# Optimization experiments

Hardware: AMD Instinct MI355X
Metric: run time of the kernel (lower is better)

## Reference

```python
import jax, jax.numpy as jnp
import numpy as np

NEG_SLOPE = 0.2  # PyG GATConv default leaky_relu slope


def gat_layer(x, src, dst, W, a_src, a_dst, bias, heads, out_ch, concat):
    """One GATConv layer (PyG semantics, shared lin for src/dst).
    x: [N, F_in]; src/dst: [E] int; W: [F_in, heads*out_ch];
    a_src/a_dst: [heads, out_ch]; bias: [heads*out_ch] or [out_ch]."""
    N = x.shape[0]
    h = (x @ W).reshape(N, heads, out_ch)              # [N, H, C]
    al_s = jnp.sum(h * a_src, axis=-1)                 # [N, H]
    al_d = jnp.sum(h * a_dst, axis=-1)                 # [N, H]
    e = jax.nn.leaky_relu(al_s[src] + al_d[dst], NEG_SLOPE)  # [E, H]
    # segment softmax over incoming edges of each destination node
    m = jax.ops.segment_max(e, dst, num_segments=N)
    m = jnp.where(jnp.isfinite(m), m, 0.0)             # nodes w/o edges
    ex = jnp.exp(e - m[dst])
    denom = jax.ops.segment_sum(ex, dst, num_segments=N)
    alpha = ex / denom[dst]                            # [E, H]; denom>0 via self-loops
    out = jax.ops.segment_sum(alpha[:, :, None] * h[src], dst, num_segments=N)  # [N,H,C]
    out = out.reshape(N, heads * out_ch) if concat else out.mean(axis=1)
    return out + bias


def setup_inputs() -> dict:
    key = jax.random.key(0)
    ks = jax.random.split(key, 10)
    N, E, F_in, Ch = 50000, 800000, 5, 64
    glorot = lambda k, shp: jax.random.uniform(
        k, shp, jnp.float32, -1.0, 1.0) * np.sqrt(6.0 / (shp[0] + shp[-1]))
    return {
        "x": jax.random.normal(ks[0], (N, F_in), jnp.float32),
        "edge_index": jax.random.randint(ks[1], (2, E), 0, N, jnp.int32),
        "W1": glorot(ks[2], (F_in, 4 * Ch)),
        "a_src1": glorot(ks[3], (4, Ch)),
        "a_dst1": glorot(ks[4], (4, Ch)),
        "b1": jnp.zeros((4 * Ch,), jnp.float32),
        "W2": glorot(ks[5], (4 * Ch, Ch)),
        "a_src2": glorot(ks[6], (1, Ch)),
        "a_dst2": glorot(ks[7], (1, Ch)),
        "b2": jnp.zeros((Ch,), jnp.float32),
    }


def reference(x, edge_index, W1, a_src1, a_dst1, b1, W2, a_src2, a_dst2, b2):
    N = x.shape[0]
    loops = jnp.arange(N, dtype=edge_index.dtype)      # PyG adds self-loops by default
    src = jnp.concatenate([edge_index[0], loops])
    dst = jnp.concatenate([edge_index[1], loops])
    h = gat_layer(x, src, dst, W1, a_src1, a_dst1, b1, heads=4, out_ch=64, concat=True)
    h = jax.nn.relu(h)
    h = gat_layer(h, src, dst, W2, a_src2, a_dst2, b2, heads=1, out_ch=64, concat=False)
    return h.mean(axis=0)                              # [64]
```

## Files before the change

### kernel.cpp

```cpp
#include <hip/hip_runtime.h>
#include <hip/hip_bf16.h>

#define NEG_SLOPE 0.2f

typedef __attribute__((ext_vector_type(8))) short short8;
typedef __attribute__((ext_vector_type(4))) float f32x4;

__device__ __forceinline__ float wave_sum64(float v) {
#pragma unroll
    for (int off = 32; off >= 1; off >>= 1) v += __shfl_xor(v, off, 64);
    return v;
}

__device__ __forceinline__ float bf2f(unsigned short u) {
    return __uint_as_float((unsigned int)u << 16);
}

__device__ __forceinline__ unsigned short f2bf(float f) {
    __hip_bfloat16 hb = __float2bfloat16(f);
    return *reinterpret_cast<unsigned short*>(&hb);
}

__global__ __launch_bounds__(256) void kb1_deg(
    const int* __restrict__ ei, int E, int Etot, int* __restrict__ deg) {
    int e = blockIdx.x * 256 + threadIdx.x;
    if (e >= Etot) return;
    int dst = (e < E) ? ei[E + e] : e - E;
    atomicAdd(&deg[dst], 1);
}

__global__ __launch_bounds__(256) void kb2_alloc(
    const int* __restrict__ deg, int N, int* __restrict__ counter,
    int* __restrict__ row_ptr, int* __restrict__ row_end,
    int* __restrict__ row_cur) {
    int n = blockIdx.x * 256 + threadIdx.x;
    int lane = threadIdx.x & 63;
    int d = (n < N) ? deg[n] : 0;
    int x = d;
#pragma unroll
    for (int off = 1; off < 64; off <<= 1) {
        int y = __shfl_up(x, off, 64);
        if (lane >= off) x += y;
    }
    int total = __shfl(x, 63, 64);
    int base = 0;
    if (lane == 63) base = atomicAdd(counter, total);
    base = __shfl(base, 63, 64);
    if (n < N) {
        int beg = base + x - d;
        row_ptr[n] = beg; row_cur[n] = beg; row_end[n] = beg + d;
    }
}

__global__ __launch_bounds__(256) void kb3_scatter(
    const int* __restrict__ ei, int E, int Etot,
    int* __restrict__ row_cur, int* __restrict__ csr_src) {
    int e = blockIdx.x * 256 + threadIdx.x;
    if (e >= Etot) return;
    int src, dst;
    if (e < E) { src = ei[e]; dst = ei[E + e]; }
    else       { src = dst = e - E; }
    int pos = atomicAdd(&row_cur[dst], 1);
    csr_src[pos] = src;
}

__global__ __launch_bounds__(256) void kw_pack(
    const float* __restrict__ W2, unsigned short* __restrict__ W2t) {
    int i = blockIdx.x * 256 + threadIdx.x;
    if (i >= 64 * 256) return;
    int c = i >> 8, k = i & 255;
    W2t[c * 256 + k] = f2bf(W2[k * 64 + c]);
}

__global__ __launch_bounds__(256) void k1_node1(
    const float* __restrict__ x, const float* __restrict__ W1,
    const float* __restrict__ a_src1, const float* __restrict__ a_dst1,
    unsigned short* __restrict__ h1b, float* __restrict__ al_s1,
    float* __restrict__ al_d1, int N) {
    int n = blockIdx.x;
    if (n >= N) return;
    int t = threadIdx.x;
    float h = 0.f;
#pragma unroll
    for (int k = 0; k < 5; ++k) h = fmaf(x[n * 5 + k], W1[k * 256 + t], h);
    int head = t >> 6, ch = t & 63;
    h1b[(size_t)n * 256 + ch * 4 + head] = f2bf(h);
    float s = wave_sum64(h * a_src1[t]);
    float d = wave_sum64(h * a_dst1[t]);
    if (ch == 0) {
        al_s1[n * 4 + head] = s;
        al_d1[n * 4 + head] = d;
    }
}

__global__ __launch_bounds__(256) void k2a_wts(
    const int* __restrict__ csr_src, const int* __restrict__ row_ptr,
    const int* __restrict__ row_end, const float* __restrict__ al_s1,
    const float* __restrict__ al_d1, float* __restrict__ ew,
    float* __restrict__ denom1, int N) {
    int wave = threadIdx.x >> 6, lane = threadIdx.x & 63;
    int n = blockIdx.x * 4 + wave;
    if (n >= N) return;
    int beg = row_ptr[n], end = row_end[n];
    const float4 ad = *reinterpret_cast<const float4*>(&al_d1[n * 4]);
    float d0 = 0.f, d1 = 0.f, d2 = 0.f, d3 = 0.f;
    for (int base = beg; base < end; base += 64) {
        int e = base + lane;
        if (e < end) {
            int src = csr_src[e];
            const float4 as = *reinterpret_cast<const float4*>(&al_s1[src * 4]);
            float v0 = as.x + ad.x, v1 = as.y + ad.y, v2 = as.z + ad.z, v3 = as.w + ad.w;
            v0 = v0 > 0.f ? v0 : NEG_SLOPE * v0;
            v1 = v1 > 0.f ? v1 : NEG_SLOPE * v1;
            v2 = v2 > 0.f ? v2 : NEG_SLOPE * v2;
            v3 = v3 > 0.f ? v3 : NEG_SLOPE * v3;
            float4 ex;
            ex.x = __expf(v0); ex.y = __expf(v1); ex.z = __expf(v2); ex.w = __expf(v3);
            *reinterpret_cast<float4*>(&ew[(size_t)e * 4]) = ex;
            d0 += ex.x; d1 += ex.y; d2 += ex.z; d3 += ex.w;
        }
    }
    d0 = wave_sum64(d0); d1 = wave_sum64(d1);
    d2 = wave_sum64(d2); d3 = wave_sum64(d3);
    if (lane == 0) {
        float4 dn = {d0, d1, d2, d3};
        *reinterpret_cast<float4*>(&denom1[n * 4]) = dn;
    }
}

__global__ __launch_bounds__(256) void k2b_gather1(
    const int* __restrict__ csr_src, const int* __restrict__ row_ptr,
    const int* __restrict__ row_end, const unsigned short* __restrict__ h1b,
    const float* __restrict__ ew, const float* __restrict__ denom1,
    const float* __restrict__ b1, unsigned short* __restrict__ x2b, int N) {
    int wave = threadIdx.x >> 6, lane = threadIdx.x & 63;
    int n = blockIdx.x * 4 + wave;
    if (n >= N) return;
    int beg = row_ptr[n], end = row_end[n];
    float a0 = 0.f, a1 = 0.f, a2 = 0.f, a3 = 0.f;
    for (int base = beg; base < end; base += 64) {
        int nn = min(64, end - base);
        int srcv = (base + lane < end) ? csr_src[base + lane] : 0;
        for (int i = 0; i < nn; ++i) {
            int src = __shfl(srcv, i, 64);
            const float4 w = *reinterpret_cast<const float4*>(&ew[(size_t)(base + i) * 4]);
            const ushort4 u = *reinterpret_cast<const ushort4*>(
                &h1b[(size_t)src * 256 + lane * 4]);
            a0 = fmaf(w.x, bf2f(u.x), a0);
            a1 = fmaf(w.y, bf2f(u.y), a1);
            a2 = fmaf(w.z, bf2f(u.z), a2);
            a3 = fmaf(w.w, bf2f(u.w), a3);
        }
    }
    const float4 dn = *reinterpret_cast<const float4*>(&denom1[n * 4]);
    unsigned short* xo = &x2b[(size_t)n * 256];
    float r;
    r = a0 / dn.x + b1[0 * 64 + lane]; xo[0 * 64 + lane] = f2bf(r > 0.f ? r : 0.f);
    r = a1 / dn.y + b1[1 * 64 + lane]; xo[1 * 64 + lane] = f2bf(r > 0.f ? r : 0.f);
    r = a2 / dn.z + b1[2 * 64 + lane]; xo[2 * 64 + lane] = f2bf(r > 0.f ? r : 0.f);
    r = a3 / dn.w + b1[3 * 64 + lane]; xo[3 * 64 + lane] = f2bf(r > 0.f ? r : 0.f);
}

__global__ __launch_bounds__(256) void k3_mfma(
    const unsigned short* __restrict__ x2b, const unsigned short* __restrict__ W2t,
    const float* __restrict__ a_src2, const float* __restrict__ a_dst2,
    float* __restrict__ h2, float* __restrict__ al_s2, float* __restrict__ al_d2,
    int N) {
    int w = threadIdx.x >> 6, l = threadIdx.x & 63;
    int m0 = blockIdx.x * 64 + w * 16;
    if (m0 >= N) return;
    int lr = l & 15, lg = l >> 4;

    short8 b0[8], b1f[8], b2f[8], b3f[8];
#pragma unroll
    for (int kk = 0; kk < 8; ++kk) {
        b0[kk]  = *reinterpret_cast<const short8*>(&W2t[(0 * 16 + lr) * 256 + kk * 32 + lg * 8]);
        b1f[kk] = *reinterpret_cast<const short8*>(&W2t[(1 * 16 + lr) * 256 + kk * 32 + lg * 8]);
        b2f[kk] = *reinterpret_cast<const short8*>(&W2t[(2 * 16 + lr) * 256 + kk * 32 + lg * 8]);
        b3f[kk] = *reinterpret_cast<const short8*>(&W2t[(3 * 16 + lr) * 256 + kk * 32 + lg * 8]);
    }
    short8 a[8];
#pragma unroll
    for (int kk = 0; kk < 8; ++kk)
        a[kk] = *reinterpret_cast<const short8*>(&x2b[(size_t)(m0 + lr) * 256 + kk * 32 + lg * 8]);

    f32x4 acc0 = {0.f, 0.f, 0.f, 0.f}, acc1 = acc0, acc2 = acc0, acc3 = acc0;
#pragma unroll
    for (int kk = 0; kk < 8; ++kk) {
        acc0 = __builtin_amdgcn_mfma_f32_16x16x32_bf16(a[kk], b0[kk],  acc0, 0, 0, 0);
        acc1 = __builtin_amdgcn_mfma_f32_16x16x32_bf16(a[kk], b1f[kk], acc1, 0, 0, 0);
        acc2 = __builtin_amdgcn_mfma_f32_16x16x32_bf16(a[kk], b2f[kk], acc2, 0, 0, 0);
        acc3 = __builtin_amdgcn_mfma_f32_16x16x32_bf16(a[kk], b3f[kk], acc3, 0, 0, 0);
    }

#pragma unroll
    for (int j = 0; j < 4; ++j) {
        float* hr = &h2[(size_t)(m0 + lg * 4 + j) * 64];
        hr[0 * 16 + lr] = acc0[j];
        hr[1 * 16 + lr] = acc1[j];
        hr[2 * 16 + lr] = acc2[j];
        hr[3 * 16 + lr] = acc3[j];
    }

    float sA0 = a_src2[0 * 16 + lr], sA1 = a_src2[1 * 16 + lr];
    float sA2 = a_src2[2 * 16 + lr], sA3 = a_src2[3 * 16 + lr];
    float sD0 = a_dst2[0 * 16 + lr], sD1 = a_dst2[1 * 16 + lr];
    float sD2 = a_dst2[2 * 16 + lr], sD3 = a_dst2[3 * 16 + lr];
    float p0 = acc0[0] * sA0 + acc1[0] * sA1 + acc2[0] * sA2 + acc3[0] * sA3;
    float p1 = acc0[1] * sA0 + acc1[1] * sA1 + acc2[1] * sA2 + acc3[1] * sA3;
    float p2 = acc0[2] * sA0 + acc1[2] * sA1 + acc2[2] * sA2 + acc3[2] * sA3;
    float p3 = acc0[3] * sA0 + acc1[3] * sA1 + acc2[3] * sA2 + acc3[3] * sA3;
    float q0 = acc0[0] * sD0 + acc1[0] * sD1 + acc2[0] * sD2 + acc3[0] * sD3;
    float q1 = acc0[1] * sD0 + acc1[1] * sD1 + acc2[1] * sD2 + acc3[1] * sD3;
    float q2 = acc0[2] * sD0 + acc1[2] * sD1 + acc2[2] * sD2 + acc3[2] * sD3;
    float q3 = acc0[3] * sD0 + acc1[3] * sD1 + acc2[3] * sD2 + acc3[3] * sD3;
#pragma unroll
    for (int off = 1; off <= 8; off <<= 1) {
        p0 += __shfl_xor(p0, off, 64); p1 += __shfl_xor(p1, off, 64);
        p2 += __shfl_xor(p2, off, 64); p3 += __shfl_xor(p3, off, 64);
        q0 += __shfl_xor(q0, off, 64); q1 += __shfl_xor(q1, off, 64);
        q2 += __shfl_xor(q2, off, 64); q3 += __shfl_xor(q3, off, 64);
    }
    if (lr == 0) {
        int r0 = m0 + lg * 4;
        al_s2[r0 + 0] = p0; al_s2[r0 + 1] = p1; al_s2[r0 + 2] = p2; al_s2[r0 + 3] = p3;
        al_d2[r0 + 0] = q0; al_d2[r0 + 1] = q1; al_d2[r0 + 2] = q2; al_d2[r0 + 3] = q3;
    }
}

__global__ __launch_bounds__(256) void k4a_wts(
    const int* __restrict__ csr_src, const int* __restrict__ row_ptr,
    const int* __restrict__ row_end, const float* __restrict__ al_s2,
    const float* __restrict__ al_d2, float* __restrict__ ew2,
    float* __restrict__ denom2, int N) {
    int wave = threadIdx.x >> 6, lane = threadIdx.x & 63;
    int n = blockIdx.x * 4 + wave;
    if (n >= N) return;
    int beg = row_ptr[n], end = row_end[n];
    float ad = al_d2[n];
    float dsum = 0.f;
    for (int base = beg; base < end; base += 64) {
        int e = base + lane;
        if (e < end) {
            int src = csr_src[e];
            float v = al_s2[src] + ad;
            v = v > 0.f ? v : NEG_SLOPE * v;
            float ex = __expf(v);
            ew2[e] = ex;
            dsum += ex;
        }
    }
    dsum = wave_sum64(dsum);
    if (lane == 0) denom2[n] = dsum;
}

__global__ __launch_bounds__(256) void k4b_gather2(
    const int* __restrict__ csr_src, const int* __restrict__ row_ptr,
    const int* __restrict__ row_end, const float* __restrict__ h2,
    const float* __restrict__ ew2, const float* __restrict__ denom2,
    float* __restrict__ o2, int N) {
    int wave = threadIdx.x >> 6, lane = threadIdx.x & 63;
    int n = blockIdx.x * 4 + wave;
    if (n >= N) return;
    int beg = row_ptr[n], end = row_end[n];
    float a = 0.f;
    for (int base = beg; base < end; base += 64) {
        int nn = min(64, end - base);
        int srcv = (base + lane < end) ? csr_src[base + lane] : 0;
        for (int i = 0; i < nn; ++i) {
            int src = __shfl(srcv, i, 64);
            float w = ew2[base + i];
            a = fmaf(w, h2[(size_t)src * 64 + lane], a);
        }
    }
    o2[(size_t)n * 64 + lane] = a / denom2[n];
}

__global__ __launch_bounds__(64) void k5_final(
    const float* __restrict__ o2, const float* __restrict__ b2,
    float* __restrict__ out, int N) {
    int lane = threadIdx.x;
    float acc = 0.f;
    for (int n = blockIdx.x; n < N; n += gridDim.x)
        acc += o2[(size_t)n * 64 + lane];
    float v = acc * (1.f / (float)N);
    if (blockIdx.x == 0) v += b2[lane];
    atomicAdd(&out[lane], v);
}

extern "C" void kernel_launch(void* const* d_in, const int* in_sizes, int n_in,
                              void* d_out, int out_size, void* d_ws, size_t ws_size,
                              hipStream_t stream) {
    const float* x   = (const float*)d_in[0];
    const int*   ei  = (const int*)d_in[1];
    const float* W1  = (const float*)d_in[2];
    const float* as1 = (const float*)d_in[3];
    const float* ad1 = (const float*)d_in[4];
    const float* b1  = (const float*)d_in[5];
    const float* W2  = (const float*)d_in[6];
    const float* as2 = (const float*)d_in[7];
    const float* ad2 = (const float*)d_in[8];
    const float* b2  = (const float*)d_in[9];
    float* out = (float*)d_out;

    const int F_in = in_sizes[2] / 256;
    const int N = in_sizes[0] / F_in;
    const int E = in_sizes[1] / 2;
    const int Etot = E + N;

    unsigned short* h1b = (unsigned short*)d_ws;
    unsigned short* x2b = h1b + (size_t)N * 256;
    float* h2    = (float*)(x2b + (size_t)N * 256);
    float* al_s1 = h2 + (size_t)N * 64;
    float* al_d1 = al_s1 + (size_t)N * 4;
    float* ew    = al_d1 + (size_t)N * 4;
    float* denom1= ew + (size_t)Etot * 4;
    unsigned short* W2t = (unsigned short*)(denom1 + (size_t)N * 4);
    int* deg     = (int*)(W2t + 64 * 256);
    int* row_cur = deg + N;
    int* row_ptr = row_cur + N;
    int* row_end = row_ptr + N;
    int* counter = row_end + N;
    int* csr_src = counter + 1;
    float* o2    = (float*)h1b;
    float* al_s2 = al_s1;
    float* al_d2 = al_d1;
    float* ew2   = ew;
    float* denom2= denom1;

    hipMemsetAsync(deg, 0, (size_t)N * sizeof(int), stream);
    hipMemsetAsync(counter, 0, sizeof(int), stream);
    hipMemsetAsync(out, 0, 64 * sizeof(float), stream);

    kb1_deg    <<<(Etot + 255) / 256, 256, 0, stream>>>(ei, E, Etot, deg);
    kb2_alloc  <<<(N + 255) / 256, 256, 0, stream>>>(deg, N, counter, row_ptr, row_end, row_cur);
    kb3_scatter<<<(Etot + 255) / 256, 256, 0, stream>>>(ei, E, Etot, row_cur, csr_src);
    kw_pack    <<<64, 256, 0, stream>>>(W2, W2t);

    k1_node1   <<<N, 256, 0, stream>>>(x, W1, as1, ad1, h1b, al_s1, al_d1, N);
    k2a_wts    <<<(N + 3) / 4, 256, 0, stream>>>(csr_src, row_ptr, row_end, al_s1, al_d1, ew, denom1, N);
    k2b_gather1<<<(N + 3) / 4, 256, 0, stream>>>(csr_src, row_ptr, row_end, h1b, ew, denom1, b1, x2b, N);
    k3_mfma    <<<(N + 63) / 64, 256, 0, stream>>>(x2b, W2t, as2, ad2, h2, al_s2, al_d2, N);
    k4a_wts    <<<(N + 3) / 4, 256, 0, stream>>>(csr_src, row_ptr, row_end, al_s2, al_d2, ew2, denom2, N);
    k4b_gather2<<<(N + 3) / 4, 256, 0, stream>>>(csr_src, row_ptr, row_end, h2, ew2, denom2, o2, N);
    k5_final   <<<256, 64, 0, stream>>>(o2, b2, out, N);
}
```

Baseline: 442.5 us.

## Aggregate raw 5-dim inputs before W1 projection and store h2 in bf16

Layer 1 is reordered by linearity: attention logits come from precomputed W1·a vectors, and the softmax-weighted sum runs over the 5-feature input x instead of the 256-wide h1. The projection through W1 is applied once per destination node. This removes the h1 materialization, the per-edge weight buffer and one gather kernel, shrinking per-edge traffic from 512 bytes to 20. Layer-2 features h2 are also stored as bf16 to halve gather bandwidth, at some cost in precision.

Result: faster. 400.4 us (-9.5%).

```diff
diff --git a/kernel.cpp b/kernel.cpp
--- a/kernel.cpp
+++ b/kernel.cpp
@@ -72,38 +72,64 @@
     W2t[c * 256 + k] = f2bf(W2[k * 64 + c]);
 }
 
-__global__ __launch_bounds__(256) void k1_node1(
-    const float* __restrict__ x, const float* __restrict__ W1,
-    const float* __restrict__ a_src1, const float* __restrict__ a_dst1,
-    unsigned short* __restrict__ h1b, float* __restrict__ al_s1,
+__global__ __launch_bounds__(256) void kpre(
+    const float* __restrict__ W1, const float* __restrict__ a_src1,
+    const float* __restrict__ a_dst1, float* __restrict__ Wa_s,
+    float* __restrict__ Wa_d) {
+    int t = threadIdx.x;
+    int h = t >> 6;
+    float a_s = a_src1[t], a_d = a_dst1[t];
+#pragma unroll
+    for (int f = 0; f < 5; ++f) {
+        float w = W1[f * 256 + t];
+        float ps = wave_sum64(w * a_s);
+        float pd = wave_sum64(w * a_d);
+        if ((t & 63) == 0) { Wa_s[f * 4 + h] = ps; Wa_d[f * 4 + h] = pd; }
+    }
+}
+
+__global__ __launch_bounds__(256) void k1p(
+    const float* __restrict__ x, const float* __restrict__ Wa_s,
+    const float* __restrict__ Wa_d, float* __restrict__ al_s1,
     float* __restrict__ al_d1, int N) {
-    int n = blockIdx.x;
+    int n = blockIdx.x * 256 + threadIdx.x;
     if (n >= N) return;
-    int t = threadIdx.x;
-    float h = 0.f;
-#pragma unroll
-    for (int k = 0; k < 5; ++k) h = fmaf(x[n * 5 + k], W1[k * 256 + t], h);
-    int head = t >> 6, ch = t & 63;
-    h1b[(size_t)n * 256 + ch * 4 + head] = f2bf(h);
-    float s = wave_sum64(h * a_src1[t]);
-    float d = wave_sum64(h * a_dst1[t]);
-    if (ch == 0) {
-        al_s1[n * 4 + head] = s;
-        al_d1[n * 4 + head] = d;
-    }
-}
-
-__global__ __launch_bounds__(256) void k2a_wts(
+    float xv[5];
+#pragma unroll
+    for (int f = 0; f < 5; ++f) xv[f] = x[n * 5 + f];
+    float4 s = {0.f, 0.f, 0.f, 0.f}, d = {0.f, 0.f, 0.f, 0.f};
+#pragma unroll
+    for (int f = 0; f < 5; ++f) {
+        s.x = fmaf(xv[f], Wa_s[f * 4 + 0], s.x);
+        s.y = fmaf(xv[f], Wa_s[f * 4 + 1], s.y);
+        s.z = fmaf(xv[f], Wa_s[f * 4 + 2], s.z);
+        s.w = fmaf(xv[f], Wa_s[f * 4 + 3], s.w);
+        d.x = fmaf(xv[f], Wa_d[f * 4 + 0], d.x);
+        d.y = fmaf(xv[f], Wa_d[f * 4 + 1], d.y);
+        d.z = fmaf(xv[f], Wa_d[f * 4 + 2], d.z);
+        d.w = fmaf(xv[f], Wa_d[f * 4 + 3], d.w);
+    }
+    *reinterpret_cast<float4*>(&al_s1[n * 4]) = s;
+    *reinterpret_cast<float4*>(&al_d1[n * 4]) = d;
+}
+
+__global__ __launch_bounds__(256) void k2_fused(
     const int* __restrict__ csr_src, const int* __restrict__ row_ptr,
-    const int* __restrict__ row_end, const float* __restrict__ al_s1,
-    const float* __restrict__ al_d1, float* __restrict__ ew,
-    float* __restrict__ denom1, int N) {
+    const int* __restrict__ row_end, const float* __restrict__ x,
+    const float* __restrict__ al_s1, const float* __restrict__ al_d1,
+    const float* __restrict__ W1, const float* __restrict__ b1,
+    unsigned short* __restrict__ x2b, int N) {
     int wave = threadIdx.x >> 6, lane = threadIdx.x & 63;
     int n = blockIdx.x * 4 + wave;
     if (n >= N) return;
     int beg = row_ptr[n], end = row_end[n];
     const float4 ad = *reinterpret_cast<const float4*>(&al_d1[n * 4]);
-    float d0 = 0.f, d1 = 0.f, d2 = 0.f, d3 = 0.f;
+    float agg[4][5];
+#pragma unroll
+    for (int h = 0; h < 4; ++h)
+#pragma unroll
+        for (int f = 0; f < 5; ++f) agg[h][f] = 0.f;
+    float dn[4] = {0.f, 0.f, 0.f, 0.f};
     for (int base = beg; base < end; base += 64) {
         int e = base + lane;
         if (e < end) {
@@ -114,58 +140,43 @@
             v1 = v1 > 0.f ? v1 : NEG_SLOPE * v1;
             v2 = v2 > 0.f ? v2 : NEG_SLOPE * v2;
             v3 = v3 > 0.f ? v3 : NEG_SLOPE * v3;
-            float4 ex;
-            ex.x = __expf(v0); ex.y = __expf(v1); ex.z = __expf(v2); ex.w = __expf(v3);
-            *reinterpret_cast<float4*>(&ew[(size_t)e * 4]) = ex;
-            d0 += ex.x; d1 += ex.y; d2 += ex.z; d3 += ex.w;
+            float ex[4];
+            ex[0] = __expf(v0); ex[1] = __expf(v1); ex[2] = __expf(v2); ex[3] = __expf(v3);
+            const float* xs = &x[(size_t)src * 5];
+            float xv[5];
+#pragma unroll
+            for (int f = 0; f < 5; ++f) xv[f] = xs[f];
+#pragma unroll
+            for (int h = 0; h < 4; ++h) {
+                dn[h] += ex[h];
+#pragma unroll
+                for (int f = 0; f < 5; ++f) agg[h][f] = fmaf(ex[h], xv[f], agg[h][f]);
+            }
         }
     }
-    d0 = wave_sum64(d0); d1 = wave_sum64(d1);
-    d2 = wave_sum64(d2); d3 = wave_sum64(d3);
-    if (lane == 0) {
-        float4 dn = {d0, d1, d2, d3};
-        *reinterpret_cast<float4*>(&denom1[n * 4]) = dn;
-    }
-}
-
-__global__ __launch_bounds__(256) void k2b_gather1(
-    const int* __restrict__ csr_src, const int* __restrict__ row_ptr,
-    const int* __restrict__ row_end, const unsigned short* __restrict__ h1b,
-    const float* __restrict__ ew, const float* __restrict__ denom1,
-    const float* __restrict__ b1, unsigned short* __restrict__ x2b, int N) {
-    int wave = threadIdx.x >> 6, lane = threadIdx.x & 63;
-    int n = blockIdx.x * 4 + wave;
-    if (n >= N) return;
-    int beg = row_ptr[n], end = row_end[n];
-    float a0 = 0.f, a1 = 0.f, a2 = 0.f, a3 = 0.f;
-    for (int base = beg; base < end; base += 64) {
-        int nn = min(64, end - base);
-        int srcv = (base + lane < end) ? csr_src[base + lane] : 0;
-        for (int i = 0; i < nn; ++i) {
-            int src = __shfl(srcv, i, 64);
-            const float4 w = *reinterpret_cast<const float4*>(&ew[(size_t)(base + i) * 4]);
-            const ushort4 u = *reinterpret_cast<const ushort4*>(
-                &h1b[(size_t)src * 256 + lane * 4]);
-            a0 = fmaf(w.x, bf2f(u.x), a0);
-            a1 = fmaf(w.y, bf2f(u.y), a1);
-            a2 = fmaf(w.z, bf2f(u.z), a2);
-            a3 = fmaf(w.w, bf2f(u.w), a3);
-        }
-    }
-    const float4 dn = *reinterpret_cast<const float4*>(&denom1[n * 4]);
+#pragma unroll
+    for (int h = 0; h < 4; ++h) {
+        dn[h] = wave_sum64(dn[h]);
+#pragma unroll
+        for (int f = 0; f < 5; ++f) agg[h][f] = wave_sum64(agg[h][f]);
+    }
     unsigned short* xo = &x2b[(size_t)n * 256];
-    float r;
-    r = a0 / dn.x + b1[0 * 64 + lane]; xo[0 * 64 + lane] = f2bf(r > 0.f ? r : 0.f);
-    r = a1 / dn.y + b1[1 * 64 + lane]; xo[1 * 64 + lane] = f2bf(r > 0.f ? r : 0.f);
-    r = a2 / dn.z + b1[2 * 64 + lane]; xo[2 * 64 + lane] = f2bf(r > 0.f ? r : 0.f);
-    r = a3 / dn.w + b1[3 * 64 + lane]; xo[3 * 64 + lane] = f2bf(r > 0.f ? r : 0.f);
+#pragma unroll
+    for (int h = 0; h < 4; ++h) {
+        float val = 0.f;
+#pragma unroll
+        for (int f = 0; f < 5; ++f)
+            val = fmaf(agg[h][f], W1[f * 256 + h * 64 + lane], val);
+        float r = val / dn[h] + b1[h * 64 + lane];
+        xo[h * 64 + lane] = f2bf(r > 0.f ? r : 0.f);
+    }
 }
 
 __global__ __launch_bounds__(256) void k3_mfma(
     const unsigned short* __restrict__ x2b, const unsigned short* __restrict__ W2t,
     const float* __restrict__ a_src2, const float* __restrict__ a_dst2,
-    float* __restrict__ h2, float* __restrict__ al_s2, float* __restrict__ al_d2,
-    int N) {
+    unsigned short* __restrict__ h2b, float* __restrict__ al_s2,
+    float* __restrict__ al_d2, int N) {
     int w = threadIdx.x >> 6, l = threadIdx.x & 63;
     int m0 = blockIdx.x * 64 + w * 16;
     if (m0 >= N) return;
@@ -195,11 +206,11 @@
 
 #pragma unroll
     for (int j = 0; j < 4; ++j) {
-        float* hr = &h2[(size_t)(m0 + lg * 4 + j) * 64];
-        hr[0 * 16 + lr] = acc0[j];
-        hr[1 * 16 + lr] = acc1[j];
-        hr[2 * 16 + lr] = acc2[j];
-        hr[3 * 16 + lr] = acc3[j];
+        unsigned short* hr = &h2b[(size_t)(m0 + lg * 4 + j) * 64];
+        hr[0 * 16 + lr] = f2bf(acc0[j]);
+        hr[1 * 16 + lr] = f2bf(acc1[j]);
+        hr[2 * 16 + lr] = f2bf(acc2[j]);
+        hr[3 * 16 + lr] = f2bf(acc3[j]);
     }
 
     float sA0 = a_src2[0 * 16 + lr], sA1 = a_src2[1 * 16 + lr];
@@ -256,7 +267,7 @@
 
 __global__ __launch_bounds__(256) void k4b_gather2(
     const int* __restrict__ csr_src, const int* __restrict__ row_ptr,
-    const int* __restrict__ row_end, const float* __restrict__ h2,
+    const int* __restrict__ row_end, const unsigned short* __restrict__ h2b,
     const float* __restrict__ ew2, const float* __restrict__ denom2,
     float* __restrict__ o2, int N) {
     int wave = threadIdx.x >> 6, lane = threadIdx.x & 63;
@@ -270,7 +281,7 @@
         for (int i = 0; i < nn; ++i) {
             int src = __shfl(srcv, i, 64);
             float w = ew2[base + i];
-            a = fmaf(w, h2[(size_t)src * 64 + lane], a);
+            a = fmaf(w, bf2f(h2b[(size_t)src * 64 + lane]), a);
         }
     }
     o2[(size_t)n * 64 + lane] = a / denom2[n];
@@ -308,25 +319,24 @@
     const int E = in_sizes[1] / 2;
     const int Etot = E + N;
 
-    unsigned short* h1b = (unsigned short*)d_ws;
-    unsigned short* x2b = h1b + (size_t)N * 256;
-    float* h2    = (float*)(x2b + (size_t)N * 256);
-    float* al_s1 = h2 + (size_t)N * 64;
+    unsigned short* x2b = (unsigned short*)d_ws;
+    unsigned short* h2b = x2b + (size_t)N * 256;
+    float* al_s1 = (float*)(h2b + (size_t)N * 64);
     float* al_d1 = al_s1 + (size_t)N * 4;
-    float* ew    = al_d1 + (size_t)N * 4;
-    float* denom1= ew + (size_t)Etot * 4;
-    unsigned short* W2t = (unsigned short*)(denom1 + (size_t)N * 4);
+    float* Wa_s  = al_d1 + (size_t)N * 4;
+    float* Wa_d  = Wa_s + 20;
+    float* ew2   = Wa_d + 20;
+    float* denom2= ew2 + (size_t)Etot;
+    unsigned short* W2t = (unsigned short*)(denom2 + N);
     int* deg     = (int*)(W2t + 64 * 256);
     int* row_cur = deg + N;
     int* row_ptr = row_cur + N;
     int* row_end = row_ptr + N;
     int* counter = row_end + N;
     int* csr_src = counter + 1;
-    float* o2    = (float*)h1b;
+    float* o2    = (float*)x2b;
     float* al_s2 = al_s1;
     float* al_d2 = al_d1;
-    float* ew2   = ew;
-    float* denom2= denom1;
 
     hipMemsetAsync(deg, 0, (size_t)N * sizeof(int), stream);
     hipMemsetAsync(counter, 0, sizeof(int), stream);
@@ -336,12 +346,12 @@
     kb2_alloc  <<<(N + 255) / 256, 256, 0, stream>>>(deg, N, counter, row_ptr, row_end, row_cur);
     kb3_scatter<<<(Etot + 255) / 256, 256, 0, stream>>>(ei, E, Etot, row_cur, csr_src);
     kw_pack    <<<64, 256, 0, stream>>>(W2, W2t);
-
-    k1_node1   <<<N, 256, 0, stream>>>(x, W1, as1, ad1, h1b, al_s1, al_d1, N);
-    k2a_wts    <<<(N + 3) / 4, 256, 0, stream>>>(csr_src, row_ptr, row_end, al_s1, al_d1, ew, denom1, N);
-    k2b_gather1<<<(N + 3) / 4, 256, 0, stream>>>(csr_src, row_ptr, row_end, h1b, ew, denom1, b1, x2b, N);
-    k3_mfma    <<<(N + 63) / 64, 256, 0, stream>>>(x2b, W2t, as2, ad2, h2, al_s2, al_d2, N);
+    kpre       <<<1, 256, 0, stream>>>(W1, as1, ad1, Wa_s, Wa_d);
+
+    k1p        <<<(N + 255) / 256, 256, 0, stream>>>(x, Wa_s, Wa_d, al_s1, al_d1, N);
+    k2_fused   <<<(N + 3) / 4, 256, 0, stream>>>(csr_src, row_ptr, row_end, x, al_s1, al_d1, W1, b1, x2b, N);
+    k3_mfma    <<<(N + 63) / 64, 256, 0, stream>>>(x2b, W2t, as2, ad2, h2b, al_s2, al_d2, N);
     k4a_wts    <<<(N + 3) / 4, 256, 0, stream>>>(csr_src, row_ptr, row_end, al_s2, al_d2, ew2, denom2, N);
-    k4b_gather2<<<(N + 3) / 4, 256, 0, stream>>>(csr_src, row_ptr, row_end, h2, ew2, denom2, o2, N);
+    k4b_gather2<<<(N + 3) / 4, 256, 0, stream>>>(csr_src, row_ptr, row_end, h2b, ew2, denom2, o2, N);
     k5_final   <<<256, 64, 0, stream>>>(o2, b2, out, N);
 }
```
